# Optimization experiments

Measured on AMD Instinct MI355X. Metric: run time of the kernel, lower is better.

## Reference

```python
import jax, jax.numpy as jnp
import numpy as np

B, T, X, Y, H = 256, 1024, 64, 64, 256


def setup_inputs() -> dict:
    key = jax.random.key(0)
    ks = jax.random.split(key, 7)
    inputs = jax.random.normal(ks[0], (B, T, X + Y), dtype=jnp.float32)
    # zero out the last quarter of timesteps so Masking(mask_value=0.0) is exercised
    tmask = (jnp.arange(T) < (3 * T) // 4).astype(jnp.float32)[None, :, None]
    inputs = inputs * tmask
    s = 0.05
    return {
        "inputs": inputs,
        "W_enc": jax.random.normal(ks[1], (X + Y, 4 * H), dtype=jnp.float32) * s,
        "U_enc": jax.random.normal(ks[2], (H, 4 * H), dtype=jnp.float32) * s,
        "b_enc": jnp.zeros((4 * H,), dtype=jnp.float32),
        "W_dec": jax.random.normal(ks[3], (X + H, 4 * H), dtype=jnp.float32) * s,
        "U_dec": jax.random.normal(ks[4], (H, 4 * H), dtype=jnp.float32) * s,
        "b_dec": jnp.zeros((4 * H,), dtype=jnp.float32),
        "W_out": jax.random.normal(ks[5], (H, Y), dtype=jnp.float32) * s,
        "b_out": jnp.zeros((Y,), dtype=jnp.float32),
        "x_dim": X,
    }


def _lstm_relu(xW_t, U, mask_t=None, return_seq=False):
    """Keras LSTM with activation='relu', recurrent_activation='sigmoid'.
    xW_t: [T,B,4H] precomputed x@W + b. mask_t: optional [T,B] bool.
    Gate order i, f, c, o (Keras). Masked steps carry (h, c) through.
    """
    Hn = U.shape[0]
    Bn = xW_t.shape[1]
    h0 = jnp.zeros((Bn, Hn), dtype=xW_t.dtype)
    c0 = jnp.zeros((Bn, Hn), dtype=xW_t.dtype)

    def step(carry, inp):
        h, c = carry
        if mask_t is None:
            xw = inp
        else:
            xw, m = inp
        z = xw + h @ U                       # [B,4H]
        i, f, g, o = jnp.split(z, 4, axis=-1)
        i = jax.nn.sigmoid(i)
        f = jax.nn.sigmoid(f)
        o = jax.nn.sigmoid(o)
        g = jax.nn.relu(g)                   # activation='relu'
        c_new = f * c + i * g
        h_new = o * jax.nn.relu(c_new)       # activation='relu' on cell output
        if mask_t is not None:
            mm = m[:, None]
            h_new = jnp.where(mm, h_new, h)
            c_new = jnp.where(mm, c_new, c)
        return (h_new, c_new), (h_new if return_seq else None)

    xs = xW_t if mask_t is None else (xW_t, mask_t)
    (h_fin, _), hs = jax.lax.scan(step, (h0, c0), xs)
    return h_fin, hs


def reference(inputs, W_enc, U_enc, b_enc, W_dec, U_dec, b_dec, W_out, b_out, x_dim):
    # Masking(mask_value=0.0): timestep valid iff any feature != 0
    mask = jnp.any(inputs != 0.0, axis=-1)                 # [B,T]
    # Encoder LSTM, return_sequences=False
    xW = jnp.einsum('bti,ij->btj', inputs, W_enc) + b_enc  # [B,T,4H]
    h_fin, _ = _lstm_relu(xW.transpose(1, 0, 2), U_enc,
                          mask_t=mask.T, return_seq=False)  # [B,H]
    # RepeatVector + concat with x part
    Tn = inputs.shape[1]
    latent_rep = jnp.broadcast_to(h_fin[:, None, :], (h_fin.shape[0], Tn, h_fin.shape[1]))
    dec_inp = jnp.concatenate([inputs[:, :, :x_dim], latent_rep], axis=-1)  # [B,T,X+H]
    # Decoder LSTM, return_sequences=True (no mask)
    xW2 = jnp.einsum('bti,ij->btj', dec_inp, W_dec) + b_dec
    _, hs = _lstm_relu(xW2.transpose(1, 0, 2), U_dec, mask_t=None, return_seq=True)  # [T,B,H]
    hs = hs.transpose(1, 0, 2)                              # [B,T,H]
    # TimeDistributed Dense(y_dim)
    return jnp.einsum('bth,hy->bty', hs, W_out) + b_out
```

## Files before the change

### kernel.cpp

```cpp
#include <hip/hip_runtime.h>


typedef __bf16 bf16x8 __attribute__((ext_vector_type(8)));
typedef float f32x4 __attribute__((ext_vector_type(4)));
typedef unsigned int uint4v __attribute__((ext_vector_type(4)));
typedef unsigned long long ull;

#define DI __device__ __forceinline__

DI unsigned short f2bf(float f) {
  unsigned int u = __float_as_uint(f);
  u += 0x7fffu + ((u >> 16) & 1u);
  return (unsigned short)(u >> 16);
}
DI float sigf(float v) { return 1.0f / (1.0f + __expf(-v)); }

union FragU { bf16x8 v; unsigned short us[8]; };
union H8 { bf16x8 v; ull u[2]; uint4v q; };

DI f32x4 mfma16(bf16x8 a, bf16x8 b, f32x4 c) {
  return __builtin_amdgcn_mfma_f32_16x16x32_bf16(a, b, c, 0, 0, 0);
}

__global__ void pack_frags(const float* __restrict__ src,
                           unsigned short* __restrict__ dst, int K, int N) {
  int KT = K >> 5, NT = N >> 4;
  int total = KT * NT * 64;
  for (int idx = blockIdx.x * blockDim.x + threadIdx.x; idx < total;
       idx += gridDim.x * blockDim.x) {
    int lane = idx & 63;
    int fi = idx >> 6;
    int nt = fi % NT;
    int kt = fi / NT;
    int r0 = kt * 32 + (lane >> 4) * 8;
    int col = nt * 16 + (lane & 15);
    unsigned int w[4];
#pragma unroll
    for (int p = 0; p < 4; ++p) {
      unsigned int lo = f2bf(src[(size_t)(r0 + 2 * p) * N + col]);
      unsigned int hi = f2bf(src[(size_t)(r0 + 2 * p + 1) * N + col]);
      w[p] = lo | (hi << 16);
    }
    *(uint4v*)(dst + (size_t)idx * 8) = (uint4v){w[0], w[1], w[2], w[3]};
  }
}

__global__ void mask_flags(const float* __restrict__ x,
                           unsigned int* __restrict__ fmask) {
  const int t = blockIdx.x;
  const int b = threadIdx.x;
  const float* p = x + ((size_t)b * 1024 + t) * 128;
  bool nz = false;
#pragma unroll 8
  for (int k = 0; k < 32; ++k) {
    float4 v = *(const float4*)(p + k * 4);
    nz = nz || v.x != 0.f || v.y != 0.f || v.z != 0.f || v.w != 0.f;
  }
  unsigned long long bal = __ballot((int)nz);
  if ((threadIdx.x & 15) == 0)
    fmask[(size_t)(b >> 4) * 1024 + t] =
        (unsigned int)((bal >> (threadIdx.x & 48)) & 0xFFFFull);
}

#define LOAD_ULDS(SRC) do {                                                 \
    _Pragma("unroll")                                                       \
    for (int vv = 0; vv < 32; ++vv) {                                       \
      int flat = vv * 256 + tid;                                            \
      int kt_ = flat >> 10, ntl = (flat >> 6) & 15, ln = flat & 63;         \
      int nt_ = (ntl >> 2) * 16 + s * 4 + (ntl & 3);                        \
      ((uint4v*)ulds)[flat] = ((const uint4v*)(SRC))[(kt_ * 64 + nt_) * 64 + ln]; \
    } } while (0)

#define EXCH_SIGNAL(FLAG, TIDX) do {                                        \
    __syncthreads();                                                        \
    if (tid == 0)                                                           \
      __hip_atomic_fetch_add(&(FLAG)[g * 1024 + (TIDX)], 1u,                \
                             __ATOMIC_RELEASE, __HIP_MEMORY_SCOPE_AGENT);   \
  } while (0)

#define EXCH_WAIT(HX, FLAG, TIDX) do {                                      \
    unsigned it_ = 0;                                                       \
    while (__hip_atomic_load(&(FLAG)[g * 1024 + (TIDX)],                    \
               __ATOMIC_RELAXED, __HIP_MEMORY_SCOPE_AGENT) < 4u) {          \
      if (++it_ > (1u << 12)) break;                                        \
    }                                                                       \
    const ull* hxr = (const ull*)((HX) + ((size_t)g * 2 + pb) * 4096);      \
    _Pragma("unroll")                                                       \
    for (int kt_ = 0; kt_ < 8; ++kt_) {                                     \
      H8 hh_;                                                               \
      hh_.u[0] = __hip_atomic_load(&hxr[(kt_ * 64 + lane) * 2],             \
                     __ATOMIC_RELAXED, __HIP_MEMORY_SCOPE_AGENT);           \
      hh_.u[1] = __hip_atomic_load(&hxr[(kt_ * 64 + lane) * 2 + 1],         \
                     __ATOMIC_RELAXED, __HIP_MEMORY_SCOPE_AGENT);           \
      hfr[kt_] = hh_.v;                                                     \
    }                                                                       \
    pb ^= 1;                                                                \
  } while (0)

__global__ __launch_bounds__(256) __attribute__((amdgpu_waves_per_eu(1, 1)))
void enc_rnn(const float* __restrict__ x,
             const unsigned short* __restrict__ Wef,
             const unsigned short* __restrict__ Uef,
             const float* __restrict__ benc,
             const unsigned int* __restrict__ fmask,
             unsigned short* __restrict__ hxE,
             unsigned int* __restrict__ flagE,
             unsigned short* __restrict__ hfin) {
  __shared__ __align__(16) unsigned short ulds[8 * 16 * 64 * 8];

  const int tid = threadIdx.x;
  const int w = tid >> 6, lane = tid & 63;
  const int l15 = lane & 15, lkg = lane >> 4;
  const int bid = blockIdx.x;
  const int s = bid >> 4, g = bid & 15;
  const int b0 = g * 16;
  int ntf[4];
#pragma unroll
  for (int G = 0; G < 4; ++G) ntf[G] = G * 16 + s * 4 + w;

  LOAD_ULDS(Uef);

  const bf16x8* Wl = (const bf16x8*)Wef + lane;
  bf16x8 wpin[4][4];
#pragma unroll
  for (int G = 0; G < 4; ++G)
#pragma unroll
    for (int kt = 0; kt < 4; ++kt) wpin[G][kt] = Wl[(kt * 64 + ntf[G]) * 64];

  float bfr[4];
#pragma unroll
  for (int G = 0; G < 4; ++G) bfr[G] = benc[ntf[G] * 16 + l15];

  float c4[4];
  unsigned short hreg[4];
  bf16x8 hfr[8];
#pragma unroll
  for (int q = 0; q < 4; ++q) { c4[q] = 0.f; hreg[q] = 0; }
  H8 z_; z_.u[0] = 0; z_.u[1] = 0;
#pragma unroll
  for (int kt = 0; kt < 8; ++kt) hfr[kt] = z_.v;

  const float* xbase = x + (size_t)(b0 + l15) * 1024 * 128 + lkg * 8;
  const unsigned int* flagp = fmask + (size_t)g * 1024;
  const int ktst = 2 * s + (w >> 1);
  const int lbase = (w & 1) * 32 + (l15 >> 3) * 16 + lkg * 4;
  const int jst = l15 & 7;
  int pb = 0;
  bool xvalid = false;
  float4 xa[4][2];

  __syncthreads();

  for (int t = 0; t < 1024; ++t) {
    const unsigned int flag_t = flagp[t];
    if (flag_t == 0u) { xvalid = false; continue; }

    if (!xvalid) {
      const float* xp = xbase + (size_t)t * 128;
#pragma unroll
      for (int kt = 0; kt < 4; ++kt) {
        xa[kt][0] = *(const float4*)(xp + kt * 32);
        xa[kt][1] = *(const float4*)(xp + kt * 32 + 4);
      }
    }

    f32x4 acc[4];
#pragma unroll
    for (int G = 0; G < 4; ++G) acc[G] = (f32x4){bfr[G], bfr[G], bfr[G], bfr[G]};

#pragma unroll
    for (int kt = 0; kt < 8; ++kt)
#pragma unroll
      for (int G = 0; G < 4; ++G) {
        bf16x8 u_ = *(const bf16x8*)&ulds[(size_t)(((kt * 16 + G * 4 + w) * 64 + lane)) * 8];
        acc[G] = mfma16(hfr[kt], u_, acc[G]);
      }

    FragU xf[4];
#pragma unroll
    for (int kt = 0; kt < 4; ++kt) {
      xf[kt].us[0] = f2bf(xa[kt][0].x); xf[kt].us[1] = f2bf(xa[kt][0].y);
      xf[kt].us[2] = f2bf(xa[kt][0].z); xf[kt].us[3] = f2bf(xa[kt][0].w);
      xf[kt].us[4] = f2bf(xa[kt][1].x); xf[kt].us[5] = f2bf(xa[kt][1].y);
      xf[kt].us[6] = f2bf(xa[kt][1].z); xf[kt].us[7] = f2bf(xa[kt][1].w);
    }
#pragma unroll
    for (int kt = 0; kt < 4; ++kt)
#pragma unroll
      for (int G = 0; G < 4; ++G) acc[G] = mfma16(xf[kt].v, wpin[G][kt], acc[G]);

    unsigned short* hxw = hxE + ((size_t)g * 2 + pb) * 4096;
#pragma unroll
    for (int q = 0; q < 4; ++q) {
      float iv = sigf(acc[0][q]);
      float fv = sigf(acc[1][q]);
      float gv = fmaxf(acc[2][q], 0.f);
      float ov = sigf(acc[3][q]);
      float cn = fv * c4[q] + iv * gv;
      float hn = ov * fmaxf(cn, 0.f);
      bool m = (flag_t >> (lkg * 4 + q)) & 1u;
      c4[q] = m ? cn : c4[q];
      unsigned short hh = m ? f2bf(hn) : hreg[q];
      hreg[q] = hh;
      __hip_atomic_store(&hxw[(ktst * 64 + lbase + q) * 8 + jst], hh,
                         __ATOMIC_RELAXED, __HIP_MEMORY_SCOPE_AGENT);
    }

    EXCH_SIGNAL(flagE, t);

    if (t < 1023) {
      const float* xq = xbase + (size_t)(t + 1) * 128;
#pragma unroll
      for (int kt = 0; kt < 4; ++kt) {
        xa[kt][0] = *(const float4*)(xq + kt * 32);
        xa[kt][1] = *(const float4*)(xq + kt * 32 + 4);
      }
      xvalid = true;
    } else xvalid = false;

    EXCH_WAIT(hxE, flagE, t);
  }

  if (w < 2) {
    int kt = 2 * s + w;
    H8 hh_; hh_.v = hfr[kt];
    *(uint4v*)&hfin[((size_t)g * 8 + kt) * 512 + lane * 8] = hh_.q;
  }
}

__global__ __launch_bounds__(256) __attribute__((amdgpu_waves_per_eu(1, 1)))
void dec_rnn(const float* __restrict__ x,
             const unsigned short* __restrict__ Wd0f,
             const unsigned short* __restrict__ WdLf,
             const unsigned short* __restrict__ Udf,
             const float* __restrict__ bdec,
             const unsigned short* __restrict__ Wof,
             const float* __restrict__ bout,
             const unsigned short* __restrict__ hfin,
             unsigned short* __restrict__ hxD,
             unsigned int* __restrict__ flagD,
             float* __restrict__ out) {
  __shared__ __align__(16) unsigned short ulds[8 * 16 * 64 * 8];

  const int tid = threadIdx.x;
  const int w = tid >> 6, lane = tid & 63;
  const int l15 = lane & 15, lkg = lane >> 4;
  const int bid = blockIdx.x;
  const int s = bid >> 4, g = bid & 15;
  const int b0 = g * 16;
  int ntf[4];
#pragma unroll
  for (int G = 0; G < 4; ++G) ntf[G] = G * 16 + s * 4 + w;

  LOAD_ULDS(Udf);

  const bf16x8* W0l = (const bf16x8*)Wd0f + lane;
  const bf16x8* WLl = (const bf16x8*)WdLf + lane;
  bf16x8 w0pin[4][2];
#pragma unroll
  for (int G = 0; G < 4; ++G)
#pragma unroll
    for (int kt = 0; kt < 2; ++kt) w0pin[G][kt] = W0l[(kt * 64 + ntf[G]) * 64];

  f32x4 lat[4];
  {
    bf16x8 ha[8];
#pragma unroll
    for (int kt = 0; kt < 8; ++kt)
      ha[kt] = *(const bf16x8*)&hfin[((size_t)g * 8 + kt) * 512 + lane * 8];
#pragma unroll
    for (int G = 0; G < 4; ++G) {
      float bd = bdec[ntf[G] * 16 + l15];
      lat[G] = (f32x4){bd, bd, bd, bd};
    }
#pragma unroll
    for (int kt = 0; kt < 8; ++kt)
#pragma unroll
      for (int G = 0; G < 4; ++G)
        lat[G] = mfma16(ha[kt], WLl[(kt * 64 + ntf[G]) * 64], lat[G]);
  }

  bf16x8 wofr[8];
  if (w == 0) {
#pragma unroll
    for (int kt = 0; kt < 8; ++kt)
      wofr[kt] = ((const bf16x8*)Wof)[(kt * 4 + s) * 64 + lane];
  }
  const float bo = bout[s * 16 + l15];

  float c4[4];
  bf16x8 hfr[8];
#pragma unroll
  for (int q = 0; q < 4; ++q) c4[q] = 0.f;
  H8 z_; z_.u[0] = 0; z_.u[1] = 0;
#pragma unroll
  for (int kt = 0; kt < 8; ++kt) hfr[kt] = z_.v;

  const float* xbase = x + (size_t)(b0 + l15) * 1024 * 128 + lkg * 8;
  const int ktst = 2 * s + (w >> 1);
  const int lbase = (w & 1) * 32 + (l15 >> 3) * 16 + lkg * 4;
  const int jst = l15 & 7;
  int pb = 0;

  float4 xa[2][2];
  xa[0][0] = *(const float4*)(xbase);      xa[0][1] = *(const float4*)(xbase + 4);
  xa[1][0] = *(const float4*)(xbase + 32); xa[1][1] = *(const float4*)(xbase + 36);

  __syncthreads();

  for (int t = 0; t < 1024; ++t) {
    f32x4 acc[4];
#pragma unroll
    for (int G = 0; G < 4; ++G) acc[G] = lat[G];

#pragma unroll
    for (int kt = 0; kt < 8; ++kt)
#pragma unroll
      for (int G = 0; G < 4; ++G) {
        bf16x8 u_ = *(const bf16x8*)&ulds[(size_t)(((kt * 16 + G * 4 + w) * 64 + lane)) * 8];
        acc[G] = mfma16(hfr[kt], u_, acc[G]);
      }

    FragU xf[2];
#pragma unroll
    for (int kt = 0; kt < 2; ++kt) {
      xf[kt].us[0] = f2bf(xa[kt][0].x); xf[kt].us[1] = f2bf(xa[kt][0].y);
      xf[kt].us[2] = f2bf(xa[kt][0].z); xf[kt].us[3] = f2bf(xa[kt][0].w);
      xf[kt].us[4] = f2bf(xa[kt][1].x); xf[kt].us[5] = f2bf(xa[kt][1].y);
      xf[kt].us[6] = f2bf(xa[kt][1].z); xf[kt].us[7] = f2bf(xa[kt][1].w);
    }
#pragma unroll
    for (int kt = 0; kt < 2; ++kt)
#pragma unroll
      for (int G = 0; G < 4; ++G) acc[G] = mfma16(xf[kt].v, w0pin[G][kt], acc[G]);

    unsigned short* hxw = hxD + ((size_t)g * 2 + pb) * 4096;
#pragma unroll
    for (int q = 0; q < 4; ++q) {
      float iv = sigf(acc[0][q]);
      float fv = sigf(acc[1][q]);
      float gv = fmaxf(acc[2][q], 0.f);
      float ov = sigf(acc[3][q]);
      float cn = fv * c4[q] + iv * gv;
      float hn = ov * fmaxf(cn, 0.f);
      c4[q] = cn;
      __hip_atomic_store(&hxw[(ktst * 64 + lbase + q) * 8 + jst], f2bf(hn),
                         __ATOMIC_RELAXED, __HIP_MEMORY_SCOPE_AGENT);
    }

    EXCH_SIGNAL(flagD, t);

    if (t > 0 && w == 0) {
      f32x4 oa = {bo, bo, bo, bo};
#pragma unroll
      for (int kt = 0; kt < 8; ++kt) oa = mfma16(hfr[kt], wofr[kt], oa);
#pragma unroll
      for (int q = 0; q < 4; ++q)
        out[((size_t)(b0 + lkg * 4 + q) * 1024 + (t - 1)) * 64 + s * 16 + l15] = oa[q];
    }
    if (t < 1023) {
      const float* xq = xbase + (size_t)(t + 1) * 128;
      xa[0][0] = *(const float4*)(xq);      xa[0][1] = *(const float4*)(xq + 4);
      xa[1][0] = *(const float4*)(xq + 32); xa[1][1] = *(const float4*)(xq + 36);
    }

    EXCH_WAIT(hxD, flagD, t);
  }

  if (w == 0) {
    f32x4 oa = {bo, bo, bo, bo};
#pragma unroll
    for (int kt = 0; kt < 8; ++kt) oa = mfma16(hfr[kt], wofr[kt], oa);
#pragma unroll
    for (int q = 0; q < 4; ++q)
      out[((size_t)(b0 + lkg * 4 + q) * 1024 + 1023) * 64 + s * 16 + l15] = oa[q];
  }
}

extern "C" void kernel_launch(void* const* d_in, const int* in_sizes, int n_in,
                              void* d_out, int out_size, void* d_ws, size_t ws_size,
                              hipStream_t stream) {
  const float* inputs = (const float*)d_in[0];
  const float* W_enc  = (const float*)d_in[1];
  const float* U_enc  = (const float*)d_in[2];
  const float* b_enc  = (const float*)d_in[3];
  const float* W_dec  = (const float*)d_in[4];
  const float* U_dec  = (const float*)d_in[5];
  const float* b_dec  = (const float*)d_in[6];
  const float* W_out  = (const float*)d_in[7];
  const float* b_out  = (const float*)d_in[8];

  char* ws = (char*)d_ws;
  unsigned short* Uef   = (unsigned short*)(ws + 0);
  unsigned short* Udf   = (unsigned short*)(ws + 524288);
  unsigned short* Wef   = (unsigned short*)(ws + 1048576);
  unsigned short* Wd0f  = (unsigned short*)(ws + 1310720);
  unsigned short* WdLf  = (unsigned short*)(ws + 1441792);
  unsigned short* Wof   = (unsigned short*)(ws + 1966080);
  unsigned short* hfin  = (unsigned short*)(ws + 1998848);
  unsigned int*   fmask = (unsigned int*)(ws + 2129920);
  unsigned int*   flagE = (unsigned int*)(ws + 2195456);
  unsigned int*   flagD = (unsigned int*)(ws + 2260992);
  unsigned short* hxE   = (unsigned short*)(ws + 2326528);
  unsigned short* hxD   = (unsigned short*)(ws + 2588672);

  hipMemsetAsync(ws + 2195456, 0, 131072, stream);

  mask_flags<<<1024, 256, 0, stream>>>(inputs, fmask);
  pack_frags<<<128, 256, 0, stream>>>(U_enc, Uef, 256, 1024);
  pack_frags<<<128, 256, 0, stream>>>(U_dec, Udf, 256, 1024);
  pack_frags<<<128, 256, 0, stream>>>(W_enc, Wef, 128, 1024);
  pack_frags<<<128, 256, 0, stream>>>(W_dec, Wd0f, 64, 1024);
  pack_frags<<<128, 256, 0, stream>>>(W_dec + 64 * 1024, WdLf, 256, 1024);
  pack_frags<<<32, 256, 0, stream>>>(W_out, Wof, 256, 64);

  enc_rnn<<<64, 256, 0, stream>>>(inputs, Wef, Uef, b_enc, fmask,
                                  hxE, flagE, hfin);
  dec_rnn<<<64, 256, 0, stream>>>(inputs, Wd0f, WdLf, Udf, b_dec, Wof, b_out,
                                  hfin, hxD, flagD, (float*)d_out);
}
```

Baseline: 5.978 ms.

## Replace flag-based h exchange with tagged words and pin U in registers

The inter-block hidden-state exchange moves from separate data writes plus an atomic counter flag to self-validating 64-bit words. Each word packs 48 bits of bf16 payload with a 16-bit step tag. That removes the release fence, the flag round trip and the flag memset. Each block stages its own h slice in LDS and only one wave polls the remote slices, which avoids a global round trip for local data. The recurrent U weights are now held in registers rather than LDS. This raises VGPR pressure and relies on tag uniqueness across steps and launches.

```diff
diff --git a/kernel.cpp b/kernel.cpp
--- a/kernel.cpp
+++ b/kernel.cpp
@@ -62,40 +62,59 @@
         (unsigned int)((bal >> (threadIdx.x & 48)) & 0xFFFFull);
 }
 
-#define LOAD_ULDS(SRC) do {                                                 \
-    _Pragma("unroll")                                                       \
-    for (int vv = 0; vv < 32; ++vv) {                                       \
-      int flat = vv * 256 + tid;                                            \
-      int kt_ = flat >> 10, ntl = (flat >> 6) & 15, ln = flat & 63;         \
-      int nt_ = (ntl >> 2) * 16 + s * 4 + (ntl & 3);                        \
-      ((uint4v*)ulds)[flat] = ((const uint4v*)(SRC))[(kt_ * 64 + nt_) * 64 + ln]; \
+#define STORE_OWN(HX) do {                                                  \
+    if (tid < 128) {                                                        \
+      const int kth = tid >> 6, word = tid & 63;                            \
+      H8 hh; hh.q = *(const uint4v*)&hstage[2 * s + kth][word][0];          \
+      const ull tg = (ull)(a + 1);                                          \
+      ull A = (hh.u[0] & 0xFFFFFFFFFFFFULL) | (tg << 48);                   \
+      ull B = ((hh.u[0] >> 48) | ((hh.u[1] & 0xFFFFFFFFULL) << 16)) |       \
+              (tg << 48);                                                   \
+      ull C = (hh.u[1] >> 32) | (tg << 32) | (tg << 48);                    \
+      ull* p_ = (HX) + (size_t)(g * 2 + (a & 1)) * 1536 +                   \
+                ((2 * s + kth) * 64 + word) * 3;                            \
+      __hip_atomic_store(p_ + 0, A, __ATOMIC_RELAXED, __HIP_MEMORY_SCOPE_AGENT); \
+      __hip_atomic_store(p_ + 1, B, __ATOMIC_RELAXED, __HIP_MEMORY_SCOPE_AGENT); \
+      __hip_atomic_store(p_ + 2, C, __ATOMIC_RELAXED, __HIP_MEMORY_SCOPE_AGENT); \
     } } while (0)
 
-#define EXCH_SIGNAL(FLAG, TIDX) do {                                        \
-    __syncthreads();                                                        \
-    if (tid == 0)                                                           \
-      __hip_atomic_fetch_add(&(FLAG)[g * 1024 + (TIDX)], 1u,                \
-                             __ATOMIC_RELEASE, __HIP_MEMORY_SCOPE_AGENT);   \
-  } while (0)
-
-#define EXCH_WAIT(HX, FLAG, TIDX) do {                                      \
-    unsigned it_ = 0;                                                       \
-    while (__hip_atomic_load(&(FLAG)[g * 1024 + (TIDX)],                    \
-               __ATOMIC_RELAXED, __HIP_MEMORY_SCOPE_AGENT) < 4u) {          \
-      if (++it_ > (1u << 12)) break;                                        \
-    }                                                                       \
-    const ull* hxr = (const ull*)((HX) + ((size_t)g * 2 + pb) * 4096);      \
-    _Pragma("unroll")                                                       \
-    for (int kt_ = 0; kt_ < 8; ++kt_) {                                     \
-      H8 hh_;                                                               \
-      hh_.u[0] = __hip_atomic_load(&hxr[(kt_ * 64 + lane) * 2],             \
-                     __ATOMIC_RELAXED, __HIP_MEMORY_SCOPE_AGENT);           \
-      hh_.u[1] = __hip_atomic_load(&hxr[(kt_ * 64 + lane) * 2 + 1],         \
-                     __ATOMIC_RELAXED, __HIP_MEMORY_SCOPE_AGENT);           \
-      hfr[kt_] = hh_.v;                                                     \
-    }                                                                       \
-    pb ^= 1;                                                                \
-  } while (0)
+#define POLL_REMOTE(HX) do {                                                \
+    if (w == 1) {                                                           \
+      const ull tg = (ull)(a + 1);                                          \
+      int rkt[6]; int nr_ = 0;                                              \
+      _Pragma("unroll")                                                     \
+      for (int s2 = 0; s2 < 4; ++s2)                                        \
+        if (s2 != s) { rkt[nr_++] = 2 * s2; rkt[nr_++] = 2 * s2 + 1; }      \
+      const ull* hb_ = (HX) + (size_t)(g * 2 + (a & 1)) * 1536;             \
+      ull R[6][3];                                                          \
+      unsigned it_ = 0;                                                     \
+      for (;;) {                                                            \
+        _Pragma("unroll")                                                   \
+        for (int r = 0; r < 6; ++r) {                                       \
+          const ull* p_ = hb_ + (rkt[r] * 64 + lane) * 3;                   \
+          R[r][0] = __hip_atomic_load(p_ + 0, __ATOMIC_RELAXED,             \
+                                      __HIP_MEMORY_SCOPE_AGENT);            \
+          R[r][1] = __hip_atomic_load(p_ + 1, __ATOMIC_RELAXED,             \
+                                      __HIP_MEMORY_SCOPE_AGENT);            \
+          R[r][2] = __hip_atomic_load(p_ + 2, __ATOMIC_RELAXED,             \
+                                      __HIP_MEMORY_SCOPE_AGENT);            \
+        }                                                                   \
+        bool ok_ = true;                                                    \
+        _Pragma("unroll")                                                   \
+        for (int r = 0; r < 6; ++r)                                         \
+          ok_ = ok_ && ((R[r][0] >> 48) == tg) && ((R[r][1] >> 48) == tg)   \
+                    && ((R[r][2] >> 48) == tg);                             \
+        if (ok_ || ++it_ > (1u << 14)) break;                               \
+      }                                                                     \
+      _Pragma("unroll")                                                     \
+      for (int r = 0; r < 6; ++r) {                                         \
+        H8 hh;                                                              \
+        hh.u[0] = (R[r][0] & 0xFFFFFFFFFFFFULL) | (R[r][1] << 48);          \
+        hh.u[1] = ((R[r][1] >> 16) & 0xFFFFFFFFULL) |                       \
+                  ((R[r][2] & 0xFFFFFFFFULL) << 32);                        \
+        *(uint4v*)&hstage[rkt[r]][lane][0] = hh.q;                          \
+      }                                                                     \
+    } } while (0)
 
 __global__ __launch_bounds__(256) __attribute__((amdgpu_waves_per_eu(1, 1)))
 void enc_rnn(const float* __restrict__ x,
@@ -103,10 +122,9 @@
              const unsigned short* __restrict__ Uef,
              const float* __restrict__ benc,
              const unsigned int* __restrict__ fmask,
-             unsigned short* __restrict__ hxE,
-             unsigned int* __restrict__ flagE,
+             ull* __restrict__ hxE,
              unsigned short* __restrict__ hfin) {
-  __shared__ __align__(16) unsigned short ulds[8 * 16 * 64 * 8];
+  __shared__ __align__(16) unsigned short hstage[8][64][8];
 
   const int tid = threadIdx.x;
   const int w = tid >> 6, lane = tid & 63;
@@ -118,9 +136,16 @@
 #pragma unroll
   for (int G = 0; G < 4; ++G) ntf[G] = G * 16 + s * 4 + w;
 
-  LOAD_ULDS(Uef);
-
   const bf16x8* Wl = (const bf16x8*)Wef + lane;
+  const bf16x8* Ul = (const bf16x8*)Uef + lane;
+  const unsigned int* flagp = fmask + (size_t)g * 1024;
+
+  bf16x8 upin[8][4];
+#pragma unroll
+  for (int kt = 0; kt < 8; ++kt)
+#pragma unroll
+    for (int G = 0; G < 4; ++G) upin[kt][G] = Ul[(kt * 64 + ntf[G]) * 64];
+
   bf16x8 wpin[4][4];
 #pragma unroll
   for (int G = 0; G < 4; ++G)
@@ -141,11 +166,10 @@
   for (int kt = 0; kt < 8; ++kt) hfr[kt] = z_.v;
 
   const float* xbase = x + (size_t)(b0 + l15) * 1024 * 128 + lkg * 8;
-  const unsigned int* flagp = fmask + (size_t)g * 1024;
-  const int ktst = 2 * s + (w >> 1);
+  const int kt_own = 2 * s + (w >> 1);
   const int lbase = (w & 1) * 32 + (l15 >> 3) * 16 + lkg * 4;
   const int jst = l15 & 7;
-  int pb = 0;
+  int a = 0;
   bool xvalid = false;
   float4 xa[4][2];
 
@@ -167,14 +191,6 @@
     f32x4 acc[4];
 #pragma unroll
     for (int G = 0; G < 4; ++G) acc[G] = (f32x4){bfr[G], bfr[G], bfr[G], bfr[G]};
-
-#pragma unroll
-    for (int kt = 0; kt < 8; ++kt)
-#pragma unroll
-      for (int G = 0; G < 4; ++G) {
-        bf16x8 u_ = *(const bf16x8*)&ulds[(size_t)(((kt * 16 + G * 4 + w) * 64 + lane)) * 8];
-        acc[G] = mfma16(hfr[kt], u_, acc[G]);
-      }
 
     FragU xf[4];
 #pragma unroll
@@ -189,7 +205,12 @@
 #pragma unroll
       for (int G = 0; G < 4; ++G) acc[G] = mfma16(xf[kt].v, wpin[G][kt], acc[G]);
 
-    unsigned short* hxw = hxE + ((size_t)g * 2 + pb) * 4096;
+#pragma unroll
+    for (int kt = 0; kt < 8; ++kt)
+#pragma unroll
+      for (int G = 0; G < 4; ++G) acc[G] = mfma16(hfr[kt], upin[kt][G], acc[G]);
+
+    unsigned short hv[4];
 #pragma unroll
     for (int q = 0; q < 4; ++q) {
       float iv = sigf(acc[0][q]);
@@ -202,11 +223,15 @@
       c4[q] = m ? cn : c4[q];
       unsigned short hh = m ? f2bf(hn) : hreg[q];
       hreg[q] = hh;
-      __hip_atomic_store(&hxw[(ktst * 64 + lbase + q) * 8 + jst], hh,
-                         __ATOMIC_RELAXED, __HIP_MEMORY_SCOPE_AGENT);
-    }
-
-    EXCH_SIGNAL(flagE, t);
+      hv[q] = hh;
+    }
+
+    __syncthreads();
+#pragma unroll
+    for (int q = 0; q < 4; ++q) hstage[kt_own][lbase + q][jst] = hv[q];
+    __syncthreads();
+
+    STORE_OWN(hxE);
 
     if (t < 1023) {
       const float* xq = xbase + (size_t)(t + 1) * 128;
@@ -218,7 +243,13 @@
       xvalid = true;
     } else xvalid = false;
 
-    EXCH_WAIT(hxE, flagE, t);
+    POLL_REMOTE(hxE);
+    __syncthreads();
+
+#pragma unroll
+    for (int kt = 0; kt < 8; ++kt)
+      hfr[kt] = *(const bf16x8*)&hstage[kt][lane][0];
+    ++a;
   }
 
   if (w < 2) {
@@ -237,10 +268,9 @@
              const unsigned short* __restrict__ Wof,
              const float* __restrict__ bout,
              const unsigned short* __restrict__ hfin,
-             unsigned short* __restrict__ hxD,
-             unsigned int* __restrict__ flagD,
+             ull* __restrict__ hxD,
              float* __restrict__ out) {
-  __shared__ __align__(16) unsigned short ulds[8 * 16 * 64 * 8];
+  __shared__ __align__(16) unsigned short hstage[8][64][8];
 
   const int tid = threadIdx.x;
   const int w = tid >> 6, lane = tid & 63;
@@ -252,10 +282,16 @@
 #pragma unroll
   for (int G = 0; G < 4; ++G) ntf[G] = G * 16 + s * 4 + w;
 
-  LOAD_ULDS(Udf);
-
   const bf16x8* W0l = (const bf16x8*)Wd0f + lane;
   const bf16x8* WLl = (const bf16x8*)WdLf + lane;
+  const bf16x8* Ul  = (const bf16x8*)Udf + lane;
+
+  bf16x8 upin[8][4];
+#pragma unroll
+  for (int kt = 0; kt < 8; ++kt)
+#pragma unroll
+    for (int G = 0; G < 4; ++G) upin[kt][G] = Ul[(kt * 64 + ntf[G]) * 64];
+
   bf16x8 w0pin[4][2];
 #pragma unroll
   for (int G = 0; G < 4; ++G)
@@ -297,10 +333,9 @@
   for (int kt = 0; kt < 8; ++kt) hfr[kt] = z_.v;
 
   const float* xbase = x + (size_t)(b0 + l15) * 1024 * 128 + lkg * 8;
-  const int ktst = 2 * s + (w >> 1);
+  const int kt_own = 2 * s + (w >> 1);
   const int lbase = (w & 1) * 32 + (l15 >> 3) * 16 + lkg * 4;
   const int jst = l15 & 7;
-  int pb = 0;
 
   float4 xa[2][2];
   xa[0][0] = *(const float4*)(xbase);      xa[0][1] = *(const float4*)(xbase + 4);
@@ -309,17 +344,10 @@
   __syncthreads();
 
   for (int t = 0; t < 1024; ++t) {
+    const int a = t;
     f32x4 acc[4];
 #pragma unroll
     for (int G = 0; G < 4; ++G) acc[G] = lat[G];
-
-#pragma unroll
-    for (int kt = 0; kt < 8; ++kt)
-#pragma unroll
-      for (int G = 0; G < 4; ++G) {
-        bf16x8 u_ = *(const bf16x8*)&ulds[(size_t)(((kt * 16 + G * 4 + w) * 64 + lane)) * 8];
-        acc[G] = mfma16(hfr[kt], u_, acc[G]);
-      }
 
     FragU xf[2];
 #pragma unroll
@@ -334,7 +362,12 @@
 #pragma unroll
       for (int G = 0; G < 4; ++G) acc[G] = mfma16(xf[kt].v, w0pin[G][kt], acc[G]);
 
-    unsigned short* hxw = hxD + ((size_t)g * 2 + pb) * 4096;
+#pragma unroll
+    for (int kt = 0; kt < 8; ++kt)
+#pragma unroll
+      for (int G = 0; G < 4; ++G) acc[G] = mfma16(hfr[kt], upin[kt][G], acc[G]);
+
+    unsigned short hv[4];
 #pragma unroll
     for (int q = 0; q < 4; ++q) {
       float iv = sigf(acc[0][q]);
@@ -344,11 +377,15 @@
       float cn = fv * c4[q] + iv * gv;
       float hn = ov * fmaxf(cn, 0.f);
       c4[q] = cn;
-      __hip_atomic_store(&hxw[(ktst * 64 + lbase + q) * 8 + jst], f2bf(hn),
-                         __ATOMIC_RELAXED, __HIP_MEMORY_SCOPE_AGENT);
-    }
-
-    EXCH_SIGNAL(flagD, t);
+      hv[q] = f2bf(hn);
+    }
+
+    __syncthreads();
+#pragma unroll
+    for (int q = 0; q < 4; ++q) hstage[kt_own][lbase + q][jst] = hv[q];
+    __syncthreads();
+
+    STORE_OWN(hxD);
 
     if (t > 0 && w == 0) {
       f32x4 oa = {bo, bo, bo, bo};
@@ -364,7 +401,12 @@
       xa[1][0] = *(const float4*)(xq + 32); xa[1][1] = *(const float4*)(xq + 36);
     }
 
-    EXCH_WAIT(hxD, flagD, t);
+    POLL_REMOTE(hxD);
+    __syncthreads();
+
+#pragma unroll
+    for (int kt = 0; kt < 8; ++kt)
+      hfr[kt] = *(const bf16x8*)&hstage[kt][lane][0];
   }
 
   if (w == 0) {
@@ -399,12 +441,8 @@
   unsigned short* Wof   = (unsigned short*)(ws + 1966080);
   unsigned short* hfin  = (unsigned short*)(ws + 1998848);
   unsigned int*   fmask = (unsigned int*)(ws + 2129920);
-  unsigned int*   flagE = (unsigned int*)(ws + 2195456);
-  unsigned int*   flagD = (unsigned int*)(ws + 2260992);
-  unsigned short* hxE   = (unsigned short*)(ws + 2326528);
-  unsigned short* hxD   = (unsigned short*)(ws + 2588672);
-
-  hipMemsetAsync(ws + 2195456, 0, 131072, stream);
+  ull*            hxE   = (ull*)(ws + 2195456);
+  ull*            hxD   = (ull*)(ws + 2588672);
 
   mask_flags<<<1024, 256, 0, stream>>>(inputs, fmask);
   pack_frags<<<128, 256, 0, stream>>>(U_enc, Uef, 256, 1024);
@@ -414,8 +452,7 @@
   pack_frags<<<128, 256, 0, stream>>>(W_dec + 64 * 1024, WdLf, 256, 1024);
   pack_frags<<<32, 256, 0, stream>>>(W_out, Wof, 256, 64);
 
-  enc_rnn<<<64, 256, 0, stream>>>(inputs, Wef, Uef, b_enc, fmask,
-                                  hxE, flagE, hfin);
+  enc_rnn<<<64, 256, 0, stream>>>(inputs, Wef, Uef, b_enc, fmask, hxE, hfin);
   dec_rnn<<<64, 256, 0, stream>>>(inputs, Wd0f, WdLf, Udf, b_dec, Wof, b_out,
-                                  hfin, hxD, flagD, (float*)d_out);
-}
+                                  hfin, hxD, (float*)d_out);
+}
```

New measurement: 4.959 ms. -17.0%, faster.
